# Optimization experiments

Measured on AMD Instinct MI355X. Metric: run time of the kernel, lower is better.

Reference implementation:

```python
import jax, jax.numpy as jnp
import numpy as np

N = 262144   # total atoms across all images
D = 128      # fingerprint (input_dimension)
H = 128      # hidden width (hiddenlayers = (128, 128))
S = 4        # number of unique element symbols (experts)
B = 1024     # number of images (segments)


def setup_inputs() -> dict:
    key = jax.random.key(0)
    ks = jax.random.split(key, 10)
    x = jax.random.normal(ks[0], (N, D), dtype=jnp.float32)
    symbol_ids = jax.random.randint(ks[1], (N,), 0, S, dtype=jnp.int32)
    image_ids = jnp.sort(jax.random.randint(ks[2], (N,), 0, B, dtype=jnp.int32))
    # per-symbol MLP params (xavier-ish scaling)
    W1 = jax.random.normal(ks[3], (S, D, H), dtype=jnp.float32) / np.sqrt(D)
    b1 = jnp.zeros((S, H), dtype=jnp.float32)
    W2 = jax.random.normal(ks[4], (S, H, H), dtype=jnp.float32) / np.sqrt(H)
    b2 = jnp.zeros((S, H), dtype=jnp.float32)
    W3 = jax.random.normal(ks[5], (S, H), dtype=jnp.float32) / np.sqrt(H)
    b3 = jnp.zeros((S,), dtype=jnp.float32)
    # per-symbol affine energy scale/shift
    slope = 1.0 + 0.1 * jax.random.normal(ks[6], (S,), dtype=jnp.float32)
    intercept = 0.1 * jax.random.normal(ks[7], (S,), dtype=jnp.float32)
    return {
        "x": x, "W1": W1, "b1": b1, "W2": W2, "b2": b2, "W3": W3, "b3": b3,
        "slope": slope, "intercept": intercept,
        "symbol_ids": symbol_ids, "image_ids": image_ids,
    }


def reference(x, W1, b1, W2, b2, W3, b3, slope, intercept, symbol_ids, image_ids):
    # Run every atom through every symbol's tiny MLP (S small), then select.
    h = jax.nn.relu(jnp.einsum('nd,sdh->nsh', x, W1) + b1)          # [N,S,H]
    h = jax.nn.relu(jnp.einsum('nsh,shk->nsk', h, W2) + b2)         # [N,S,H]
    e = jnp.einsum('nsh,sh->ns', h, W3) + b3                         # [N,S] atomic energy per expert
    e = slope * e + intercept                                        # per-symbol affine
    e_atom = jnp.take_along_axis(e, symbol_ids[:, None].astype(jnp.int32), axis=1)[:, 0]  # [N] routed
    # per-image energy = sum of atomic energies in that image
    return jax.ops.segment_sum(e_atom, image_ids, num_segments=B)    # [B]
```

## Files before the change

kernel.cpp:

```cpp
#include <hip/hip_runtime.h>
#include <hip/hip_bf16.h>
#include <stdint.h>

typedef _Float16 f16x8 __attribute__((ext_vector_type(8)));
typedef __fp16 hf2 __attribute__((ext_vector_type(2)));
typedef float f32x4 __attribute__((ext_vector_type(4)));
typedef unsigned int u32x4 __attribute__((ext_vector_type(4)));
typedef unsigned int u32x2 __attribute__((ext_vector_type(2)));

#define N_ATOMS 262144
#define NSYM 4
#define NIMG 1024

__global__ void hist_kernel(const int* __restrict__ sym, int* __restrict__ wbh) {
  int b = blockIdx.x;
  int i = b * 256 + threadIdx.x;
  int lane = threadIdx.x & 63, wave = threadIdx.x >> 6;
  __shared__ int wcnt[4][NSYM];
  int s = sym[i];
#pragma unroll
  for (int t = 0; t < NSYM; ++t) {
    unsigned long long m = __ballot(s == t);
    if (lane == 0) wcnt[wave][t] = __popcll(m);
  }
  __syncthreads();
  if (threadIdx.x < NSYM)
    wbh[b * 4 + threadIdx.x] = wcnt[0][threadIdx.x] + wcnt[1][threadIdx.x] +
                               wcnt[2][threadIdx.x] + wcnt[3][threadIdx.x];
}

__global__ void fusedprep_kernel(const int* __restrict__ wbh, int* __restrict__ bases,
                                 int* __restrict__ offs, int* __restrict__ perm,
                                 const float* __restrict__ W1, const float* __restrict__ W2,
                                 unsigned short* __restrict__ wt) {
  if (blockIdx.x >= 1) {
    int idx = (blockIdx.x - 1) * 256 + threadIdx.x;
    int t = idx >> 14;
    int layer = t >> 2, s = t & 3;
    int rem = idx & 16383;
    int h = rem >> 7, u = rem & 127;
    int gs = u >> 3, j = u & 7;
    int d = ((gs ^ (h & 7)) << 3) + j;
    const float* W = layer ? W2 : W1;
    _Float16 hv = (_Float16)W[(s * 128 + d) * 128 + h];
    wt[t * 16384 + h * 128 + u] = __builtin_bit_cast(unsigned short, hv);
    return;
  }
  __shared__ int wtot[4][NSYM];
  __shared__ int offsh[NSYM + 1];
  __shared__ int totsh[NSYM];
  int t = threadIdx.x, lane = t & 63, wave = t >> 6;
  int pre[4][NSYM];
  int sum[NSYM] = {0, 0, 0, 0};
#pragma unroll
  for (int k = 0; k < 4; ++k)
#pragma unroll
    for (int s2 = 0; s2 < NSYM; ++s2) {
      pre[k][s2] = sum[s2];
      sum[s2] += wbh[(t * 4 + k) * 4 + s2];
    }
  int inc[NSYM] = {sum[0], sum[1], sum[2], sum[3]};
  for (int d = 1; d < 64; d <<= 1) {
#pragma unroll
    for (int s2 = 0; s2 < NSYM; ++s2) {
      int v = __shfl_up(inc[s2], d);
      if (lane >= d) inc[s2] += v;
    }
  }
  if (lane == 63)
#pragma unroll
    for (int s2 = 0; s2 < NSYM; ++s2) wtot[wave][s2] = inc[s2];
  __syncthreads();
  int wb[NSYM];
#pragma unroll
  for (int s2 = 0; s2 < NSYM; ++s2) {
    wb[s2] = 0;
    for (int w = 0; w < wave; ++w) wb[s2] += wtot[w][s2];
  }
  if (t == 255)
#pragma unroll
    for (int s2 = 0; s2 < NSYM; ++s2) totsh[s2] = wb[s2] + inc[s2];
  __syncthreads();
  if (t == 0) {
    int o = 0;
    offsh[0] = 0; offs[0] = 0;
    for (int s2 = 0; s2 < NSYM; ++s2) {
      o += (totsh[s2] + 255) & ~255;
      offsh[s2 + 1] = o; offs[s2 + 1] = o;
    }
  }
  __syncthreads();
#pragma unroll
  for (int k = 0; k < 4; ++k)
#pragma unroll
    for (int s2 = 0; s2 < NSYM; ++s2)
      bases[(t * 4 + k) * 4 + s2] = offsh[s2] + wb[s2] + (inc[s2] - sum[s2]) + pre[k][s2];
  for (int s2 = 0; s2 < NSYM; ++s2) {
    int lo = offsh[s2] + totsh[s2], hi = offsh[s2 + 1];
    for (int i = lo + t; i < hi; i += 256) perm[i] = -1;
  }
}

__global__ void scatter_kernel(const int* __restrict__ sym, const int* __restrict__ bases,
                               int* __restrict__ perm) {
  int b = blockIdx.x;
  int i = b * 256 + threadIdx.x;
  int lane = threadIdx.x & 63, wave = threadIdx.x >> 6;
  __shared__ int wcnt[4][NSYM];
  int s = sym[i];
  unsigned long long mymask = 0;
#pragma unroll
  for (int t = 0; t < NSYM; ++t) {
    unsigned long long m = __ballot(s == t);
    if (lane == 0) wcnt[wave][t] = __popcll(m);
    if (s == t) mymask = m;
  }
  __syncthreads();
  int off = bases[b * 4 + s];
  for (int w = 0; w < wave; ++w) off += wcnt[w][s];
  off += __popcll(mymask & ((1ull << lane) - 1ull));
  perm[off] = i;
}

__global__ __launch_bounds__(512, 2) void mlp_gemm(
    const float* __restrict__ x, const unsigned short* __restrict__ wt,
    const int* __restrict__ perm, const int* __restrict__ offs,
    const float* __restrict__ b1, const float* __restrict__ b2,
    const float* __restrict__ W3, const float* __restrict__ b3,
    const float* __restrict__ slope, const float* __restrict__ intercept,
    float* __restrict__ e_atom) {
  extern __shared__ char lds[];

  int s = blockIdx.x >> 6;
  int kblk = blockIdx.x & 63;
  int base = offs[s];
  int T = (offs[s + 1] - base) >> 8;

  int tid = threadIdx.x;
  int wave = tid >> 6, lane = tid & 63;
  int r0 = lane & 15, chunk = lane >> 4;
  int l32 = lane & 31, half = lane >> 5;
  char* stage = lds + 65536 + wave * 8192;

  const unsigned short* w1p = wt + (size_t)(0 + s) * 16384;
  const unsigned short* w2p = wt + (size_t)(4 + s) * 16384;

#pragma unroll
  for (int it = 0; it < 8; ++it) {
    int gb = it * 512 + wave * 64;
    const unsigned short* src = (gb >= 2048) ? (w2p + (size_t)(gb - 2048 + lane) * 8)
                                             : (w1p + (size_t)(gb + lane) * 8);
    __builtin_amdgcn_global_load_lds((const unsigned int*)src,
                                     (unsigned int*)(lds + (size_t)gb * 16), 16, 0, 0);
  }

  float b1v[8], b2v[8], w3v[8];
#pragma unroll
  for (int cf = 0; cf < 8; ++cf) {
    b1v[cf] = b1[s * 128 + cf * 16 + r0];
    b2v[cf] = b2[s * 128 + cf * 16 + r0];
    w3v[cf] = W3[s * 128 + cf * 16 + r0];
  }
  float sl = slope[s], ic = intercept[s], bb = b3[s];

  int cur_perm = (kblk < T) ? perm[base + (kblk << 8) + wave * 32 + l32] : -1;
  float4 raw[16];
#pragma unroll
  for (int it = 0; it < 16; ++it) {
    int atom = __shfl(cur_perm, it * 2 + half);
    raw[it] = *(const float4*)(x + (size_t)(atom < 0 ? 0 : atom) * 128 + l32 * 4);
  }

  __syncthreads();

  f32x4 zero4 = {0.f, 0.f, 0.f, 0.f};

  for (int t = kblk; t < T; t += 64) {
    int tn = t + 64;
    int nperm = -1;
    if (tn < T) nperm = perm[base + (tn << 8) + wave * 32 + l32];

#pragma unroll
    for (int it = 0; it < 16; ++it) {
      int row = it * 2 + half;
      hf2 p0 = __builtin_amdgcn_cvt_pkrtz(raw[it].x, raw[it].y);
      hf2 p1 = __builtin_amdgcn_cvt_pkrtz(raw[it].z, raw[it].w);
      u32x2 w2 = {__builtin_bit_cast(unsigned int, p0), __builtin_bit_cast(unsigned int, p1)};
      int gs = (l32 >> 1) ^ (row & 7);
      *(u32x2*)(stage + row * 256 + gs * 16 + (l32 & 1) * 8) = w2;
    }
    f16x8 ah[8];
#pragma unroll
    for (int rf = 0; rf < 2; ++rf)
#pragma unroll
      for (int kk = 0; kk < 4; ++kk) {
        int row = rf * 16 + r0;
        ah[rf * 4 + kk] = *(const f16x8*)(stage + row * 256 +
                                          (((kk * 4 + chunk) ^ (row & 7)) << 4));
      }

    f32x4 acc[2][8];
#pragma unroll
    for (int i = 0; i < 2; ++i)
#pragma unroll
      for (int j = 0; j < 8; ++j) acc[i][j] = zero4;

#pragma unroll
    for (int k = 0; k < 4; ++k)
#pragma unroll
      for (int cf = 0; cf < 8; ++cf) {
        int row = cf * 16 + r0;
        f16x8 bh = *(const f16x8*)(lds + row * 256 +
                                   ((((k * 4 + chunk)) << 4) ^ ((row & 7) << 4)));
        acc[0][cf] = __builtin_amdgcn_mfma_f32_16x16x32_f16(ah[k], bh, acc[0][cf], 0, 0, 0);
        acc[1][cf] = __builtin_amdgcn_mfma_f32_16x16x32_f16(ah[4 + k], bh, acc[1][cf], 0, 0, 0);
      }

#pragma unroll
    for (int hp2 = 0; hp2 < 2; ++hp2) {
#pragma unroll
      for (int cf4 = 0; cf4 < 4; ++cf4) {
        int cf = hp2 * 4 + cf4;
        float bias = b1v[cf];
        int colp = cf4 * 16 + r0;
#pragma unroll
        for (int rf = 0; rf < 2; ++rf)
#pragma unroll
          for (int rr = 0; rr < 4; ++rr) {
            int row = rf * 16 + chunk * 4 + rr;
            float v = fmaxf(acc[rf][cf][rr] + bias, 0.f);
            unsigned short h = __builtin_bit_cast(unsigned short, (_Float16)v);
            int cc = colp ^ (chunk << 4) ^ (rr << 2);
            *(unsigned int*)(stage + row * 256 + cc * 4) = ((unsigned int)h << 16) | h;
          }
      }
#pragma unroll
      for (int kk2 = 0; kk2 < 2; ++kk2) {
        int kk = hp2 * 2 + kk2;
#pragma unroll
        for (int rf = 0; rf < 2; ++rf) {
          int row = rf * 16 + r0;
          int xr3 = ((r0 >> 2) << 4) ^ ((r0 & 3) << 2);
          int c0 = kk2 * 32 + chunk * 8;
          u32x4 pa = *(const u32x4*)(stage + row * 256 + (c0 ^ xr3) * 4);
          u32x4 pb = *(const u32x4*)(stage + row * 256 + ((c0 + 4) ^ xr3) * 4);
          unsigned int h01 = (pa[0] >> 16) | (pa[1] & 0xffff0000u);
          unsigned int h23 = (pa[2] >> 16) | (pa[3] & 0xffff0000u);
          unsigned int h45 = (pb[0] >> 16) | (pb[1] & 0xffff0000u);
          unsigned int h67 = (pb[2] >> 16) | (pb[3] & 0xffff0000u);
          u32x4 hq = {h01, h23, h45, h67};
          ah[rf * 4 + kk] = __builtin_bit_cast(f16x8, hq);
        }
      }
    }

    if (tn < T) {
#pragma unroll
      for (int it = 0; it < 16; ++it) {
        int atom = __shfl(nperm, it * 2 + half);
        raw[it] = *(const float4*)(x + (size_t)(atom < 0 ? 0 : atom) * 128 + l32 * 4);
      }
    }

#pragma unroll
    for (int i = 0; i < 2; ++i)
#pragma unroll
      for (int j = 0; j < 8; ++j) acc[i][j] = zero4;

#pragma unroll
    for (int k = 0; k < 4; ++k)
#pragma unroll
      for (int cf = 0; cf < 8; ++cf) {
        int row = cf * 16 + r0;
        f16x8 bh = *(const f16x8*)(lds + 32768 + row * 256 +
                                   ((((k * 4 + chunk)) << 4) ^ ((row & 7) << 4)));
        acc[0][cf] = __builtin_amdgcn_mfma_f32_16x16x32_f16(ah[k], bh, acc[0][cf], 0, 0, 0);
        acc[1][cf] = __builtin_amdgcn_mfma_f32_16x16x32_f16(ah[4 + k], bh, acc[1][cf], 0, 0, 0);
      }

    float p[2][4] = {{0.f, 0.f, 0.f, 0.f}, {0.f, 0.f, 0.f, 0.f}};
#pragma unroll
    for (int cf = 0; cf < 8; ++cf)
#pragma unroll
      for (int rf = 0; rf < 2; ++rf)
#pragma unroll
        for (int rr = 0; rr < 4; ++rr)
          p[rf][rr] += fmaxf(acc[rf][cf][rr] + b2v[cf], 0.f) * w3v[cf];
#pragma unroll
    for (int m = 1; m < 16; m <<= 1)
#pragma unroll
      for (int rf = 0; rf < 2; ++rf)
#pragma unroll
        for (int rr = 0; rr < 4; ++rr) p[rf][rr] += __shfl_xor(p[rf][rr], m);

    int atom_w[2][4];
#pragma unroll
    for (int rf = 0; rf < 2; ++rf)
#pragma unroll
      for (int rr = 0; rr < 4; ++rr)
        atom_w[rf][rr] = __shfl(cur_perm, rf * 16 + chunk * 4 + rr);

    if (r0 == 0) {
#pragma unroll
      for (int rf = 0; rf < 2; ++rf)
#pragma unroll
        for (int rr = 0; rr < 4; ++rr)
          if (atom_w[rf][rr] >= 0)
            e_atom[atom_w[rf][rr]] = sl * (p[rf][rr] + bb) + ic;
    }

    cur_perm = nperm;
  }
}

__global__ void segsum_kernel(const float* __restrict__ e_atom, const int* __restrict__ img,
                              float* __restrict__ out, int n) {
  int b = blockIdx.x;
  int lo = 0, hi = n;
  while (lo < hi) { int m = (lo + hi) >> 1; if (img[m] < b) lo = m + 1; else hi = m; }
  int lo2 = lo, hi2 = n;
  while (lo2 < hi2) { int m = (lo2 + hi2) >> 1; if (img[m] < b + 1) lo2 = m + 1; else hi2 = m; }
  float sum = 0.f;
  for (int i = lo + threadIdx.x; i < lo2; i += blockDim.x) sum += e_atom[i];
  for (int m = 32; m; m >>= 1) sum += __shfl_down(sum, m);
  __shared__ float part[4];
  int lane = threadIdx.x & 63, wave = threadIdx.x >> 6;
  if (lane == 0) part[wave] = sum;
  __syncthreads();
  if (threadIdx.x == 0) out[b] = part[0] + part[1] + part[2] + part[3];
}

extern "C" void kernel_launch(void* const* d_in, const int* in_sizes, int n_in,
                              void* d_out, int out_size, void* d_ws, size_t ws_size,
                              hipStream_t stream) {
  const float* x         = (const float*)d_in[0];
  const float* W1        = (const float*)d_in[1];
  const float* b1        = (const float*)d_in[2];
  const float* W2        = (const float*)d_in[3];
  const float* b2        = (const float*)d_in[4];
  const float* W3        = (const float*)d_in[5];
  const float* b3        = (const float*)d_in[6];
  const float* slope     = (const float*)d_in[7];
  const float* intercept = (const float*)d_in[8];
  const int* sym         = (const int*)d_in[9];
  const int* img         = (const int*)d_in[10];

  char* ws = (char*)d_ws;
  int* wbh    = (int*)ws;
  int* bases  = (int*)(ws + 16384);
  int* offs   = (int*)(ws + 32768);
  int* perm   = (int*)(ws + 32832);
  float* e_atom = (float*)(ws + 32832 + 1052672);
  unsigned short* wt = (unsigned short*)(ws + 32832 + 1052672 + 1048576);

  hist_kernel<<<1024, 256, 0, stream>>>(sym, wbh);
  fusedprep_kernel<<<513, 256, 0, stream>>>(wbh, bases, offs, perm, W1, W2, wt);
  scatter_kernel<<<1024, 256, 0, stream>>>(sym, bases, perm);
  mlp_gemm<<<256, 512, 131072, stream>>>(x, wt, perm, offs, b1, b2,
                                         W3, b3, slope, intercept, e_atom);
  segsum_kernel<<<NIMG, 256, 0, stream>>>(e_atom, img, (float*)d_out, N_ATOMS);
}
```

Measured before the change: 63.27 us.

## Keep layer-1 activations in registers by transposing MFMA and re-laying out W2

Swaps the MFMA operand order in layer 1 so each lane's accumulator holds the hidden-unit values it needs as the A operand of layer 2. The ReLU'd activations are packed to fp16 directly in registers instead of going through a shared-memory staging transpose. The W2 prep layout is permuted to match, and layer 2 uses 16x16x16 MFMAs on the register-resident operands. This removes LDS writes, reads and bit-unpacking per tile, at the cost of twice as many smaller MFMA instructions in layer 2.

```diff
diff --git a/kernel.cpp b/kernel.cpp
--- a/kernel.cpp
+++ b/kernel.cpp
@@ -3,6 +3,7 @@
 #include <stdint.h>
 
 typedef _Float16 f16x8 __attribute__((ext_vector_type(8)));
+typedef _Float16 f16x4 __attribute__((ext_vector_type(4)));
 typedef __fp16 hf2 __attribute__((ext_vector_type(2)));
 typedef float f32x4 __attribute__((ext_vector_type(4)));
 typedef unsigned int u32x4 __attribute__((ext_vector_type(4)));
@@ -36,14 +37,25 @@
   if (blockIdx.x >= 1) {
     int idx = (blockIdx.x - 1) * 256 + threadIdx.x;
     int t = idx >> 14;
-    int layer = t >> 2, s = t & 3;
     int rem = idx & 16383;
-    int h = rem >> 7, u = rem & 127;
-    int gs = u >> 3, j = u & 7;
-    int d = ((gs ^ (h & 7)) << 3) + j;
-    const float* W = layer ? W2 : W1;
-    _Float16 hv = (_Float16)W[(s * 128 + d) * 128 + h];
-    wt[t * 16384 + h * 128 + u] = __builtin_bit_cast(unsigned short, hv);
+    if (t < 4) {
+      int s = t;
+      int h = rem >> 7, u = rem & 127;
+      int gs = u >> 3, j = u & 7;
+      int d = ((gs ^ (h & 7)) << 3) + j;
+      _Float16 hv = (_Float16)W1[(s * 128 + d) * 128 + h];
+      wt[t * 16384 + h * 128 + u] = __builtin_bit_cast(unsigned short, hv);
+    } else {
+      int s = t - 4;
+      int h2 = rem >> 7, q = rem & 127;
+      int Up = q >> 3, e = q & 7;
+      int U = Up ^ (h2 & 7);
+      int p = U >> 2, c = U & 3;
+      int cf = 2 * p + (e >> 2), j = e & 3;
+      int h1 = cf * 16 + c * 4 + j;
+      _Float16 hv = (_Float16)W2[(s * 128 + h1) * 128 + h2];
+      wt[t * 16384 + h2 * 128 + q] = __builtin_bit_cast(unsigned short, hv);
+    }
     return;
   }
   __shared__ int wtot[4][NSYM];
@@ -154,10 +166,11 @@
                                      (unsigned int*)(lds + (size_t)gb * 16), 16, 0, 0);
   }
 
-  float b1v[8], b2v[8], w3v[8];
+  float4 b1q[8];
+  float b2v[8], w3v[8];
 #pragma unroll
   for (int cf = 0; cf < 8; ++cf) {
-    b1v[cf] = b1[s * 128 + cf * 16 + r0];
+    b1q[cf] = *(const float4*)(b1 + s * 128 + cf * 16 + chunk * 4);
     b2v[cf] = b2[s * 128 + cf * 16 + r0];
     w3v[cf] = W3[s * 128 + cf * 16 + r0];
   }
@@ -212,47 +225,26 @@
         int row = cf * 16 + r0;
         f16x8 bh = *(const f16x8*)(lds + row * 256 +
                                    ((((k * 4 + chunk)) << 4) ^ ((row & 7) << 4)));
-        acc[0][cf] = __builtin_amdgcn_mfma_f32_16x16x32_f16(ah[k], bh, acc[0][cf], 0, 0, 0);
-        acc[1][cf] = __builtin_amdgcn_mfma_f32_16x16x32_f16(ah[4 + k], bh, acc[1][cf], 0, 0, 0);
-      }
-
-#pragma unroll
-    for (int hp2 = 0; hp2 < 2; ++hp2) {
-#pragma unroll
-      for (int cf4 = 0; cf4 < 4; ++cf4) {
-        int cf = hp2 * 4 + cf4;
-        float bias = b1v[cf];
-        int colp = cf4 * 16 + r0;
-#pragma unroll
-        for (int rf = 0; rf < 2; ++rf)
-#pragma unroll
-          for (int rr = 0; rr < 4; ++rr) {
-            int row = rf * 16 + chunk * 4 + rr;
-            float v = fmaxf(acc[rf][cf][rr] + bias, 0.f);
-            unsigned short h = __builtin_bit_cast(unsigned short, (_Float16)v);
-            int cc = colp ^ (chunk << 4) ^ (rr << 2);
-            *(unsigned int*)(stage + row * 256 + cc * 4) = ((unsigned int)h << 16) | h;
-          }
-      }
-#pragma unroll
-      for (int kk2 = 0; kk2 < 2; ++kk2) {
-        int kk = hp2 * 2 + kk2;
-#pragma unroll
-        for (int rf = 0; rf < 2; ++rf) {
-          int row = rf * 16 + r0;
-          int xr3 = ((r0 >> 2) << 4) ^ ((r0 & 3) << 2);
-          int c0 = kk2 * 32 + chunk * 8;
-          u32x4 pa = *(const u32x4*)(stage + row * 256 + (c0 ^ xr3) * 4);
-          u32x4 pb = *(const u32x4*)(stage + row * 256 + ((c0 + 4) ^ xr3) * 4);
-          unsigned int h01 = (pa[0] >> 16) | (pa[1] & 0xffff0000u);
-          unsigned int h23 = (pa[2] >> 16) | (pa[3] & 0xffff0000u);
-          unsigned int h45 = (pb[0] >> 16) | (pb[1] & 0xffff0000u);
-          unsigned int h67 = (pb[2] >> 16) | (pb[3] & 0xffff0000u);
-          u32x4 hq = {h01, h23, h45, h67};
-          ah[rf * 4 + kk] = __builtin_bit_cast(f16x8, hq);
-        }
-      }
-    }
+        acc[0][cf] = __builtin_amdgcn_mfma_f32_16x16x32_f16(bh, ah[k], acc[0][cf], 0, 0, 0);
+        acc[1][cf] = __builtin_amdgcn_mfma_f32_16x16x32_f16(bh, ah[4 + k], acc[1][cf], 0, 0, 0);
+      }
+
+    u32x2 ah2[2][8];
+#pragma unroll
+    for (int rf = 0; rf < 2; ++rf)
+#pragma unroll
+      for (int cf = 0; cf < 8; ++cf) {
+        float v0 = fmaxf(acc[rf][cf][0] + b1q[cf].x, 0.f);
+        float v1 = fmaxf(acc[rf][cf][1] + b1q[cf].y, 0.f);
+        float v2 = fmaxf(acc[rf][cf][2] + b1q[cf].z, 0.f);
+        float v3 = fmaxf(acc[rf][cf][3] + b1q[cf].w, 0.f);
+        unsigned int h0 = __builtin_bit_cast(unsigned short, (_Float16)v0);
+        unsigned int h1 = __builtin_bit_cast(unsigned short, (_Float16)v1);
+        unsigned int h2 = __builtin_bit_cast(unsigned short, (_Float16)v2);
+        unsigned int h3 = __builtin_bit_cast(unsigned short, (_Float16)v3);
+        u32x2 pk = {h0 | (h1 << 16), h2 | (h3 << 16)};
+        ah2[rf][cf] = pk;
+      }
 
     if (tn < T) {
 #pragma unroll
@@ -262,36 +254,45 @@
       }
     }
 
+    f32x4 acc2[2][8];
 #pragma unroll
     for (int i = 0; i < 2; ++i)
 #pragma unroll
-      for (int j = 0; j < 8; ++j) acc[i][j] = zero4;
-
-#pragma unroll
-    for (int k = 0; k < 4; ++k)
-#pragma unroll
-      for (int cf = 0; cf < 8; ++cf) {
-        int row = cf * 16 + r0;
-        f16x8 bh = *(const f16x8*)(lds + 32768 + row * 256 +
-                                   ((((k * 4 + chunk)) << 4) ^ ((row & 7) << 4)));
-        acc[0][cf] = __builtin_amdgcn_mfma_f32_16x16x32_f16(ah[k], bh, acc[0][cf], 0, 0, 0);
-        acc[1][cf] = __builtin_amdgcn_mfma_f32_16x16x32_f16(ah[4 + k], bh, acc[1][cf], 0, 0, 0);
-      }
-
-    float p[2][4] = {{0.f, 0.f, 0.f, 0.f}, {0.f, 0.f, 0.f, 0.f}};
-#pragma unroll
-    for (int cf = 0; cf < 8; ++cf)
+      for (int j = 0; j < 8; ++j) acc2[i][j] = zero4;
+
+#pragma unroll
+    for (int p = 0; p < 4; ++p)
+#pragma unroll
+      for (int t2 = 0; t2 < 8; ++t2) {
+        int row = t2 * 16 + r0;
+        f16x8 w = *(const f16x8*)(lds + 32768 + row * 256 +
+                                  (((p * 4 + chunk) ^ (r0 & 7)) << 4));
+        f16x4 blo = __builtin_shufflevector(w, w, 0, 1, 2, 3);
+        f16x4 bhi = __builtin_shufflevector(w, w, 4, 5, 6, 7);
+        acc2[0][t2] = __builtin_amdgcn_mfma_f32_16x16x16f16(
+            __builtin_bit_cast(f16x4, ah2[0][2 * p]), blo, acc2[0][t2], 0, 0, 0);
+        acc2[1][t2] = __builtin_amdgcn_mfma_f32_16x16x16f16(
+            __builtin_bit_cast(f16x4, ah2[1][2 * p]), blo, acc2[1][t2], 0, 0, 0);
+        acc2[0][t2] = __builtin_amdgcn_mfma_f32_16x16x16f16(
+            __builtin_bit_cast(f16x4, ah2[0][2 * p + 1]), bhi, acc2[0][t2], 0, 0, 0);
+        acc2[1][t2] = __builtin_amdgcn_mfma_f32_16x16x16f16(
+            __builtin_bit_cast(f16x4, ah2[1][2 * p + 1]), bhi, acc2[1][t2], 0, 0, 0);
+      }
+
+    float p2[2][4] = {{0.f, 0.f, 0.f, 0.f}, {0.f, 0.f, 0.f, 0.f}};
+#pragma unroll
+    for (int t2 = 0; t2 < 8; ++t2)
 #pragma unroll
       for (int rf = 0; rf < 2; ++rf)
 #pragma unroll
         for (int rr = 0; rr < 4; ++rr)
-          p[rf][rr] += fmaxf(acc[rf][cf][rr] + b2v[cf], 0.f) * w3v[cf];
+          p2[rf][rr] += fmaxf(acc2[rf][t2][rr] + b2v[t2], 0.f) * w3v[t2];
 #pragma unroll
     for (int m = 1; m < 16; m <<= 1)
 #pragma unroll
       for (int rf = 0; rf < 2; ++rf)
 #pragma unroll
-        for (int rr = 0; rr < 4; ++rr) p[rf][rr] += __shfl_xor(p[rf][rr], m);
+        for (int rr = 0; rr < 4; ++rr) p2[rf][rr] += __shfl_xor(p2[rf][rr], m);
 
     int atom_w[2][4];
 #pragma unroll
@@ -306,7 +307,7 @@
 #pragma unroll
         for (int rr = 0; rr < 4; ++rr)
           if (atom_w[rf][rr] >= 0)
-            e_atom[atom_w[rf][rr]] = sl * (p[rf][rr] + bb) + ic;
+            e_atom[atom_w[rf][rr]] = sl * (p2[rf][rr] + bb) + ic;
     }
 
     cur_perm = nperm;
```

Measured after the change: 62.79 us (median of 2 runs). Within noise of the previous version (-0.8%).
